# Kernel optimization log

Hardware: AMD Instinct MI355X
Metric: run time of the kernel (lower is better)

## Reference

```python
import jax, jax.numpy as jnp
import numpy as np

B, S, C_IN, C_OUT = 8, 2048, 512, 512

def setup_inputs() -> dict:
    key = jax.random.key(0)
    k1, k2, k3, k4 = jax.random.split(key, 4)
    sc = 1.0 / np.sqrt(C_IN)
    return {
        "x": jax.random.normal(k1, (B, S, C_IN), dtype=jnp.float32),
        "Wq": jax.random.normal(k2, (C_OUT, C_IN), dtype=jnp.float32) * sc,
        "Wk": jax.random.normal(k3, (C_OUT, C_IN), dtype=jnp.float32) * sc,
        "Wv": jax.random.normal(k4, (C_OUT, C_IN), dtype=jnp.float32) * sc,
    }

def reference(x, Wq, Wk, Wv):
    # x: [B,S,Cin]; weights [Cout,Cin] (torch Linear convention, no bias)
    C = Wq.shape[0]
    dk = jnp.sqrt(jnp.float32(1.0) / C)  # torch: sqrt(1/out_features)
    q = jnp.einsum('bsi,oi->bso', x, Wq)
    k = jnp.einsum('bsi,oi->bso', x, Wk)
    v = jnp.einsum('bsi,oi->bso', x, Wv)
    phi_q = jax.nn.elu(q * dk) + 1.0
    phi_k = jax.nn.elu(k * dk) + 1.0
    b = x.shape[0]
    mem0 = jnp.zeros((b, C, C), x.dtype)   # running sum of phi_k v^T
    zeta0 = jnp.zeros((b, C), x.dtype)     # running sum of phi_k
    def step(carry, inp):
        mem, zeta = carry
        pq, pk, vv = inp                    # each [B,C]
        dm = pk[:, :, None] * vv[:, None, :]              # [B,C,C]
        scale = jnp.einsum('bc,bc->b', pq, pk + zeta) + 1e-5
        num = jnp.einsum('bc,bcd->bd', pq, dm + mem)
        y = num / scale[:, None]
        # state updates are under torch.no_grad -> detach
        new_mem = jax.lax.stop_gradient(mem + dm)
        new_zeta = jax.lax.stop_gradient(zeta + pk)
        return (new_mem, new_zeta), y
    xs = (phi_q.transpose(1, 0, 2), phi_k.transpose(1, 0, 2), v.transpose(1, 0, 2))
    _, ys = jax.lax.scan(step, (mem0, zeta0), xs)  # ys: [S,B,C]
    return ys.transpose(1, 0, 2)                   # [B,S,C]
```

## Files before the change

### kernel.cpp

```cpp
#include <hip/hip_runtime.h>


constexpr int Bn  = 8;
constexpr int Sn  = 2048;
constexpr int Cn  = 512;
constexpr int Tn  = 128;
constexpr int NCn = 16;
constexpr float DKf = 0.04419417382415922f;

typedef __attribute__((ext_vector_type(8))) short bf16x8;
typedef __attribute__((ext_vector_type(4))) float f32x4;

__device__ __forceinline__ unsigned short f2bf(float f) {
  unsigned u = __float_as_uint(f);
  u = (u + 0x7fffu + ((u >> 16) & 1u)) >> 16;
  return (unsigned short)u;
}
__device__ __forceinline__ float bf2f(unsigned short h) {
  return __uint_as_float(((unsigned)h) << 16);
}
__device__ __forceinline__ float phi_f(float u) {
  float s = u * DKf;
  return s > 0.0f ? s + 1.0f : __expf(s);
}

__global__ __launch_bounds__(256) void k_cast(
    const float* __restrict__ x, const float* __restrict__ Wq,
    const float* __restrict__ Wk, const float* __restrict__ Wv,
    unsigned short* __restrict__ xb, unsigned short* __restrict__ Wb)
{
  const int bid = blockIdx.x;
  const float* src;
  unsigned short* dst;
  size_t i8;
  if (bid < 4096) {
    i8 = ((size_t)bid * 256 + threadIdx.x) * 8;
    src = x; dst = xb;
  } else {
    const size_t f = ((size_t)(bid - 4096) * 256 + threadIdx.x) * 8;
    const int z = (int)(f >> 18);
    src = (z == 0) ? Wq : (z == 1 ? Wk : Wv);
    dst = Wb + ((size_t)z << 18);
    i8 = f & ((1u << 18) - 1);
  }
  float4 a = *(const float4*)&src[i8];
  float4 b = *(const float4*)&src[i8 + 4];
  uint4 o;
  o.x = (unsigned)f2bf(a.x) | ((unsigned)f2bf(a.y) << 16);
  o.y = (unsigned)f2bf(a.z) | ((unsigned)f2bf(a.w) << 16);
  o.z = (unsigned)f2bf(b.x) | ((unsigned)f2bf(b.y) << 16);
  o.w = (unsigned)f2bf(b.z) | ((unsigned)f2bf(b.w) << 16);
  *(uint4*)&dst[i8] = o;
}

__device__ __forceinline__ void stage128x64(const unsigned short* __restrict__ g,
                                            int ld, unsigned short* lds,
                                            int wid, int lane) {
#pragma unroll
  for (int e = 0; e < 4; ++e) {
    const int row = e * 32 + wid * 8 + (lane >> 3);
    const int ks  = (lane & 7) ^ (row & 7);
    const unsigned short* src = g + (size_t)row * ld + ks * 8;
    unsigned short* dst = lds + (size_t)(e * 256 + wid * 64) * 8;
    __builtin_amdgcn_global_load_lds(
        (const __attribute__((address_space(1))) void*)src,
        (__attribute__((address_space(3))) void*)dst, 16, 0, 0);
  }
}

__global__ __launch_bounds__(256) void k_proj(
    const unsigned short* __restrict__ xb, const unsigned short* __restrict__ Wb,
    unsigned short* __restrict__ PQ, unsigned short* __restrict__ PK,
    unsigned short* __restrict__ PKt, unsigned short* __restrict__ Vt,
    float* __restrict__ zsum)
{
  __shared__ unsigned short Al[2 * 8192], Bl[2 * 8192];
  __shared__ float zbuf[2][128];
  const int bid = blockIdx.x;
  const int xcd = bid & 7, idx = bid >> 3;
  const int n = idx & 3, z = (idx >> 2) % 3, mloc = idx / 12;
  const int n0 = n * 128, m0 = (xcd * 16 + mloc) * 128;
  const int t = threadIdx.x, wid = t >> 6, lane = t & 63;
  const int wm = wid >> 1, wn = wid & 1;
  const int fr = lane & 15, kb = lane >> 4;
  f32x4 acc[4][4];
  const f32x4 zero = {0.f, 0.f, 0.f, 0.f};
#pragma unroll
  for (int m = 0; m < 4; ++m)
#pragma unroll
    for (int nn = 0; nn < 4; ++nn) acc[m][nn] = zero;

  const unsigned short* Ag = xb + (size_t)m0 * Cn;
  const unsigned short* Bg = Wb + (size_t)z * Cn * Cn + (size_t)n0 * Cn;

  stage128x64(Ag, Cn, Al, wid, lane);
  stage128x64(Bg, Cn, Bl, wid, lane);
  int cur = 0;
  for (int kt = 0; kt < 8; ++kt) {
    const int nxt = cur ^ 1;
    if (kt + 1 < 8) {
      stage128x64(Ag + (kt + 1) * 64, Cn, Al + nxt * 8192, wid, lane);
      stage128x64(Bg + (kt + 1) * 64, Cn, Bl + nxt * 8192, wid, lane);
      asm volatile("s_waitcnt vmcnt(8)" ::: "memory");
    } else {
      asm volatile("s_waitcnt vmcnt(0)" ::: "memory");
    }
    __builtin_amdgcn_s_barrier();
    asm volatile("" ::: "memory");
    const unsigned short* Ac = Al + cur * 8192;
    const unsigned short* Bc = Bl + cur * 8192;
#pragma unroll
    for (int kk = 0; kk < 2; ++kk) {
      bf16x8 af[4], bf[4];
#pragma unroll
      for (int m = 0; m < 4; ++m) {
        const int r = wm * 64 + m * 16 + fr;
        af[m] = *(const bf16x8*)&Ac[r * 64 + (((kk * 4 + kb) ^ (r & 7)) << 3)];
      }
#pragma unroll
      for (int nn = 0; nn < 4; ++nn) {
        const int r = wn * 64 + nn * 16 + fr;
        bf[nn] = *(const bf16x8*)&Bc[r * 64 + (((kk * 4 + kb) ^ (r & 7)) << 3)];
      }
      __builtin_amdgcn_s_setprio(1);
#pragma unroll
      for (int m = 0; m < 4; ++m)
#pragma unroll
        for (int nn = 0; nn < 4; ++nn)
          acc[m][nn] = __builtin_amdgcn_mfma_f32_16x16x32_bf16(af[m], bf[nn], acc[m][nn], 0, 0, 0);
      __builtin_amdgcn_s_setprio(0);
    }
    __builtin_amdgcn_s_barrier();
    asm volatile("" ::: "memory");
    cur = nxt;
  }

  float ps[4] = {0.f, 0.f, 0.f, 0.f};
#pragma unroll
  for (int m = 0; m < 4; ++m)
#pragma unroll
    for (int nn = 0; nn < 4; ++nn) {
      const int row0 = m0 + wm * 64 + m * 16 + ((lane >> 4) << 2);
      const int col  = n0 + wn * 64 + nn * 16 + fr;
      f32x4 v = acc[m][nn];
      if (z == 0) {
#pragma unroll
        for (int j = 0; j < 4; ++j)
          PQ[(size_t)(row0 + j) * Cn + col] = f2bf(phi_f(v[j]));
      } else if (z == 1) {
        ushort4 p;
#pragma unroll
        for (int j = 0; j < 4; ++j) {
          unsigned short u = f2bf(phi_f(v[j]));
          PK[(size_t)(row0 + j) * Cn + col] = u;
          (&p.x)[j] = u;
          ps[nn] += bf2f(u);
        }
        const int b = row0 >> 11, tq = row0 & (Sn - 1);
        *(ushort4*)&PKt[((size_t)b * Cn + col) * Sn + tq] = p;
      } else {
        ushort4 p;
#pragma unroll
        for (int j = 0; j < 4; ++j) (&p.x)[j] = f2bf(v[j]);
        const int b = row0 >> 11, tq = row0 & (Sn - 1);
        *(ushort4*)&Vt[((size_t)b * Cn + col) * Sn + tq] = p;
      }
    }

  if (z == 1) {
#pragma unroll
    for (int nn = 0; nn < 4; ++nn) {
      float v = ps[nn];
      v += __shfl_xor(v, 16); v += __shfl_xor(v, 32);
      if (lane < 16) zbuf[wm][wn * 64 + nn * 16 + lane] = v;
    }
    __syncthreads();
    if (t < 128) {
      const int b = m0 >> 11, ch = (m0 >> 7) & 15;
      zsum[((size_t)b * NCn + ch) * Cn + n0 + t] = zbuf[0][t] + zbuf[1][t];
    }
  }
}

__device__ __forceinline__ void stageA64(const unsigned short* __restrict__ g,
                                         unsigned short* lds, int wid, int lane) {
  const int row = wid * 16 + (lane >> 2);
  const int ks  = (lane & 3) ^ ((row >> 1) & 3);
  __builtin_amdgcn_global_load_lds(
      (const __attribute__((address_space(1))) void*)(g + (size_t)row * Cn + ks * 8),
      (__attribute__((address_space(3))) void*)(lds + wid * 512), 16, 0, 0);
}
__device__ __forceinline__ void stageB128(const unsigned short* __restrict__ g,
                                          unsigned short* lds, int wid, int lane) {
#pragma unroll
  for (int e = 0; e < 2; ++e) {
    const int row = e * 64 + wid * 16 + (lane >> 2);
    const int ks  = (lane & 3) ^ ((row >> 1) & 3);
    __builtin_amdgcn_global_load_lds(
        (const __attribute__((address_space(1))) void*)(g + (size_t)row * Cn + ks * 8),
        (__attribute__((address_space(3))) void*)(lds + e * 2048 + wid * 512),
        16, 0, 0);
  }
}

__device__ __forceinline__ void stage64x128(const unsigned short* __restrict__ g,
                                            int ld, unsigned short* lds,
                                            int wid, int lane) {
#pragma unroll
  for (int i = 0; i < 4; ++i) {
    const int row = wid * 16 + i * 4 + (lane >> 4);
    const int s   = (lane & 15) ^ (row & 7);
    const unsigned short* src = g + (size_t)row * ld + s * 8;
    unsigned short* dst = lds + (size_t)(wid * 16 + i * 4) * 128;
    __builtin_amdgcn_global_load_lds(
        (const __attribute__((address_space(1))) void*)src,
        (__attribute__((address_space(3))) void*)dst, 16, 0, 0);
  }
}

__global__ __launch_bounds__(256) void k_gk(
    const unsigned short* __restrict__ PQ, const unsigned short* __restrict__ PK,
    const float* __restrict__ zsum,
    unsigned short* __restrict__ Abuf, float* __restrict__ scale,
    const unsigned short* __restrict__ PKt, const unsigned short* __restrict__ Vt,
    unsigned short* __restrict__ Mpre)
{
  __shared__ unsigned short smem[32768];
  const int t = threadIdx.x, wid = t >> 6, lane = t & 63;
  const int fr = lane & 15, kb = lane >> 4;
  const f32x4 zero = {0.f, 0.f, 0.f, 0.f};

  if (blockIdx.x < 512) {
    unsigned short* Al = smem;
    unsigned short* Bl = smem + 16384;
    const int bid = blockIdx.x;
    const int b = bid & 7, idx = bid >> 3;
    const int d0 = (idx & 7) * 64, c0 = (idx >> 3) * 64;
    const int wm = wid >> 1, wn = wid & 1;
    f32x4 acc[2][2];
#pragma unroll
    for (int m = 0; m < 2; ++m)
#pragma unroll
      for (int n = 0; n < 2; ++n) acc[m][n] = zero;
    const unsigned short* Ag = PKt + ((size_t)b * Cn + c0) * Sn;
    const unsigned short* Bg = Vt  + ((size_t)b * Cn + d0) * Sn;
    stage64x128(Ag, Sn, Al, wid, lane);
    stage64x128(Bg, Sn, Bl, wid, lane);
    int cur = 0;
    for (int ch = 0; ch < NCn; ++ch) {
      const int nxt = cur ^ 1;
      if (ch + 1 < NCn) {
        stage64x128(Ag + (ch + 1) * Tn, Sn, Al + nxt * 8192, wid, lane);
        stage64x128(Bg + (ch + 1) * Tn, Sn, Bl + nxt * 8192, wid, lane);
        asm volatile("s_waitcnt vmcnt(8)" ::: "memory");
      } else {
        asm volatile("s_waitcnt vmcnt(0)" ::: "memory");
      }
      __builtin_amdgcn_s_barrier();
      asm volatile("" ::: "memory");
      if (ch > 0) {
#pragma unroll
        for (int m = 0; m < 2; ++m)
#pragma unroll
          for (int n = 0; n < 2; ++n) {
            const int c_row = c0 + wm * 32 + m * 16 + (kb << 2);
            const int d     = d0 + wn * 32 + n * 16 + fr;
            ushort4 p;
#pragma unroll
            for (int j = 0; j < 4; ++j) (&p.x)[j] = f2bf(acc[m][n][j]);
            *(ushort4*)&Mpre[((size_t)(b * NCn + ch) * Cn + d) * Cn + c_row] = p;
          }
      }
      const unsigned short* Ac = Al + cur * 8192;
      const unsigned short* Bc = Bl + cur * 8192;
      __builtin_amdgcn_s_setprio(1);
#pragma unroll
      for (int kt = 0; kt < 4; ++kt) {
        bf16x8 af[2], bf[2];
#pragma unroll
        for (int m = 0; m < 2; ++m) {
          const int r = wm * 32 + m * 16 + fr;
          af[m] = *(const bf16x8*)&Ac[r * 128 + (((kt * 4 + kb) ^ (r & 7)) << 3)];
        }
#pragma unroll
        for (int n = 0; n < 2; ++n) {
          const int r = wn * 32 + n * 16 + fr;
          bf[n] = *(const bf16x8*)&Bc[r * 128 + (((kt * 4 + kb) ^ (r & 7)) << 3)];
        }
#pragma unroll
        for (int m = 0; m < 2; ++m)
#pragma unroll
          for (int n = 0; n < 2; ++n)
            acc[m][n] = __builtin_amdgcn_mfma_f32_16x16x32_bf16(af[m], bf[n], acc[m][n], 0, 0, 0);
      }
      __builtin_amdgcn_s_setprio(0);
      __builtin_amdgcn_s_barrier();
      asm volatile("" ::: "memory");
      cur = nxt;
    }
  } else {
    unsigned short* Asl = smem;
    unsigned short* Bsl = smem + 6144;
    float* rsmem = (float*)(smem + 18432);
    float* zpl   = rsmem + 256;
    const int g = blockIdx.x - 512;
    const int i0 = (g & 1) * 64, ch = (g >> 1) & 15, b = g >> 5;
    const unsigned short* Aq = PQ + ((size_t)(b * Sn + ch * Tn + i0)) * Cn;
    const unsigned short* Bk = PK + ((size_t)(b * Sn + ch * Tn)) * Cn;
    f32x4 acc[4][2];
#pragma unroll
    for (int m = 0; m < 4; ++m)
#pragma unroll
      for (int n = 0; n < 2; ++n) acc[m][n] = zero;

    stageA64(Aq, Asl, wid, lane);
    stageB128(Bk, Bsl, wid, lane);
    stageA64(Aq + 32, Asl + 2048, wid, lane);
    stageB128(Bk + 32, Bsl + 4096, wid, lane);
    int cur = 0;
    for (int kt = 0; kt < 16; ++kt) {
      if (kt + 2 < 16) {
        const int nx2 = (cur + 2 >= 3) ? cur - 1 : cur + 2;
        stageA64(Aq + (kt + 2) * 32, Asl + nx2 * 2048, wid, lane);
        stageB128(Bk + (kt + 2) * 32, Bsl + nx2 * 4096, wid, lane);
        asm volatile("s_waitcnt vmcnt(6)" ::: "memory");
      } else if (kt + 1 < 16) {
        asm volatile("s_waitcnt vmcnt(3)" ::: "memory");
      } else {
        asm volatile("s_waitcnt vmcnt(0)" ::: "memory");
      }
      __builtin_amdgcn_s_barrier();
      asm volatile("" ::: "memory");
      const unsigned short* Ac = Asl + cur * 2048;
      const unsigned short* Bc = Bsl + cur * 4096;
      bf16x8 af[4], bf[2];
#pragma unroll
      for (int m = 0; m < 4; ++m) {
        const int r = m * 16 + fr;
        af[m] = *(const bf16x8*)&Ac[r * 32 + ((kb ^ ((r >> 1) & 3)) << 3)];
      }
#pragma unroll
      for (int n = 0; n < 2; ++n) {
        const int c = wid * 32 + n * 16 + fr;
        bf[n] = *(const bf16x8*)&Bc[c * 32 + ((kb ^ ((c >> 1) & 3)) << 3)];
      }
      __builtin_amdgcn_s_setprio(1);
#pragma unroll
      for (int m = 0; m < 4; ++m)
#pragma unroll
        for (int n = 0; n < 2; ++n)
          acc[m][n] = __builtin_amdgcn_mfma_f32_16x16x32_bf16(af[m], bf[n], acc[m][n], 0, 0, 0);
      __builtin_amdgcn_s_setprio(0);
      __builtin_amdgcn_s_barrier();
      asm volatile("" ::: "memory");
      cur = (cur + 1 >= 3) ? 0 : cur + 1;
    }

    float rsum[4][4];
#pragma unroll
    for (int m = 0; m < 4; ++m)
#pragma unroll
      for (int j = 0; j < 4; ++j) rsum[m][j] = 0.f;
#pragma unroll
    for (int m = 0; m < 4; ++m)
#pragma unroll
      for (int n = 0; n < 2; ++n) {
        f32x4 v = acc[m][n];
#pragma unroll
        for (int j = 0; j < 4; ++j) {
          const int row_g = i0 + m * 16 + kb * 4 + j;
          const int col   = wid * 32 + n * 16 + fr;
          unsigned short u = (col <= row_g) ? f2bf(v[j]) : 0;
          Abuf[((size_t)(b * NCn + ch) * Tn + row_g) * Tn + col] = u;
          rsum[m][j] += bf2f(u);
        }
      }
#pragma unroll
    for (int m = 0; m < 4; ++m)
#pragma unroll
      for (int j = 0; j < 4; ++j) {
        float r = rsum[m][j];
        r += __shfl_xor(r, 1); r += __shfl_xor(r, 2);
        r += __shfl_xor(r, 4); r += __shfl_xor(r, 8);
        if (fr == 0) rsmem[wid * 64 + m * 16 + kb * 4 + j] = r;
      }
#pragma unroll
    for (int e = 0; e < 2; ++e) {
      const int c = t + e * 256;
      float s = 0.f;
      for (int ch2 = 0; ch2 < ch; ++ch2)
        s += zsum[((size_t)b * NCn + ch2) * Cn + c];
      zpl[c] = s;
    }
    __syncthreads();
    const int row = t >> 2, q4 = (t & 3) * 128;
    const unsigned short* pq = Aq + (size_t)row * Cn + q4;
    float dacc = 0.f;
    for (int i = 0; i < 128; i += 8) {
      uint4 q = *(const uint4*)(pq + i);
      dacc += bf2f((unsigned short)(q.x & 0xffff)) * zpl[q4 + i + 0]
            + bf2f((unsigned short)(q.x >> 16))    * zpl[q4 + i + 1]
            + bf2f((unsigned short)(q.y & 0xffff)) * zpl[q4 + i + 2]
            + bf2f((unsigned short)(q.y >> 16))    * zpl[q4 + i + 3]
            + bf2f((unsigned short)(q.z & 0xffff)) * zpl[q4 + i + 4]
            + bf2f((unsigned short)(q.z >> 16))    * zpl[q4 + i + 5]
            + bf2f((unsigned short)(q.w & 0xffff)) * zpl[q4 + i + 6]
            + bf2f((unsigned short)(q.w >> 16))    * zpl[q4 + i + 7];
    }
    dacc += __shfl_xor(dacc, 1);
    dacc += __shfl_xor(dacc, 2);
    if ((t & 3) == 0)
      scale[(size_t)b * Sn + ch * Tn + i0 + row] =
          rsmem[0 * 64 + row] + rsmem[1 * 64 + row] +
          rsmem[2 * 64 + row] + rsmem[3 * 64 + row] + dacc + 1e-5f;
  }
}

__device__ __forceinline__ void stage128x32(const unsigned short* __restrict__ g,
                                            int ld, unsigned short* lds,
                                            int wid, int lane) {
#pragma unroll
  for (int cc = 0; cc < 2; ++cc) {
    const int row = cc * 64 + wid * 16 + (lane >> 2);
    const int ks  = (lane & 3) ^ ((row >> 1) & 3);
    const unsigned short* src = g + (size_t)row * ld + ks * 8;
    unsigned short* dst = lds + (size_t)(cc * 256 + wid * 64) * 8;
    __builtin_amdgcn_global_load_lds(
        (const __attribute__((address_space(1))) void*)src,
        (__attribute__((address_space(3))) void*)dst, 16, 0, 0);
  }
}

__global__ __launch_bounds__(256) void k_avinter(
    const unsigned short* __restrict__ Abuf, const unsigned short* __restrict__ Vt,
    const unsigned short* __restrict__ PQ, const unsigned short* __restrict__ Mpre,
    const float* __restrict__ scale, float* __restrict__ out)
{
  __shared__ unsigned short Al[3 * 128 * 32], Bl[3 * 128 * 32];
  const int bid = blockIdx.x;
  const int logical = (bid & 7) * 64 + (bid >> 3);
  const int d0 = (logical & 3) * 128;
  const int ch = (logical >> 2) & 15;
  const int b  = logical >> 6;
  const int t0 = ch * Tn;
  const int t = threadIdx.x, wid = t >> 6, lane = t & 63;
  const int wm = wid >> 1, wn = wid & 1;
  const int fr = lane & 15, kb = lane >> 4;
  f32x4 acc[4][4];
  const f32x4 zero = {0.f, 0.f, 0.f, 0.f};
#pragma unroll
  for (int m = 0; m < 4; ++m)
#pragma unroll
    for (int n = 0; n < 4; ++n) acc[m][n] = zero;

  const unsigned short* Aintra = Abuf + (size_t)(b * NCn + ch) * Tn * Tn;
  const unsigned short* Bintra = Vt + ((size_t)b * Cn + d0) * Sn + t0;
  const unsigned short* Ainter = PQ + ((size_t)b * Sn + t0) * Cn;
  const unsigned short* Binter = Mpre + ((size_t)(b * NCn + ch) * Cn + d0) * Cn;
  auto srcA = [&](int kt) { return (kt < 4) ? Aintra + kt * 32 : Ainter + (kt - 4) * 32; };
  auto srcB = [&](int kt) { return (kt < 4) ? Bintra + kt * 32 : Binter + (kt - 4) * 32; };
  auto ldA  = [&](int kt) { return (kt < 4) ? Tn : Cn; };
  auto ldB  = [&](int kt) { return (kt < 4) ? Sn : Cn; };
  const int nkt = (ch > 0) ? 20 : 4;

  stage128x32(srcA(0), ldA(0), Al, wid, lane);
  stage128x32(srcB(0), ldB(0), Bl, wid, lane);
  stage128x32(srcA(1), ldA(1), Al + 4096, wid, lane);
  stage128x32(srcB(1), ldB(1), Bl + 4096, wid, lane);
  int cur = 0;
  for (int kt = 0; kt < nkt; ++kt) {
    if (kt + 2 < nkt) {
      const int nx2 = (cur + 2 >= 3) ? cur - 1 : cur + 2;
      stage128x32(srcA(kt + 2), ldA(kt + 2), Al + nx2 * 4096, wid, lane);
      stage128x32(srcB(kt + 2), ldB(kt + 2), Bl + nx2 * 4096, wid, lane);
      asm volatile("s_waitcnt vmcnt(8)" ::: "memory");
    } else if (kt + 1 < nkt) {
      asm volatile("s_waitcnt vmcnt(4)" ::: "memory");
    } else {
      asm volatile("s_waitcnt vmcnt(0)" ::: "memory");
    }
    __builtin_amdgcn_s_barrier();
    asm volatile("" ::: "memory");
    const unsigned short* Ac = Al + cur * 4096;
    const unsigned short* Bc = Bl + cur * 4096;
    bf16x8 af[4], bf[4];
#pragma unroll
    for (int m = 0; m < 4; ++m) {
      const int r = wm * 64 + m * 16 + fr;
      af[m] = *(const bf16x8*)&Ac[r * 32 + ((kb ^ ((r >> 1) & 3)) << 3)];
    }
#pragma unroll
    for (int n = 0; n < 4; ++n) {
      const int r = wn * 64 + n * 16 + fr;
      bf[n] = *(const bf16x8*)&Bc[r * 32 + ((kb ^ ((r >> 1) & 3)) << 3)];
    }
    __builtin_amdgcn_s_setprio(1);
#pragma unroll
    for (int m = 0; m < 4; ++m)
#pragma unroll
      for (int n = 0; n < 4; ++n)
        acc[m][n] = __builtin_amdgcn_mfma_f32_16x16x32_bf16(af[m], bf[n], acc[m][n], 0, 0, 0);
    __builtin_amdgcn_s_setprio(0);
    __builtin_amdgcn_s_barrier();
    asm volatile("" ::: "memory");
    cur = (cur + 1 >= 3) ? 0 : cur + 1;
  }

#pragma unroll
  for (int m = 0; m < 4; ++m)
#pragma unroll
    for (int n = 0; n < 4; ++n) {
      const int row0 = t0 + wm * 64 + m * 16 + ((lane >> 4) << 2);
      const int col  = d0 + wn * 64 + n * 16 + (lane & 15);
      f32x4 v = acc[m][n];
#pragma unroll
      for (int j = 0; j < 4; ++j) {
        const size_t sidx = (size_t)b * Sn + row0 + j;
        out[sidx * Cn + col] = v[j] / scale[sidx];
      }
    }
}

extern "C" void kernel_launch(void* const* d_in, const int* in_sizes, int n_in,
                              void* d_out, int out_size, void* d_ws, size_t ws_size,
                              hipStream_t stream)
{
  const float* x  = (const float*)d_in[0];
  const float* Wq = (const float*)d_in[1];
  const float* Wk = (const float*)d_in[2];
  const float* Wv = (const float*)d_in[3];
  float* out = (float*)d_out;

  unsigned short* xb   = (unsigned short*)d_ws;
  unsigned short* Wb   = xb   + (size_t)Bn * Sn * Cn;
  unsigned short* PQ   = Wb   + (size_t)3 * Cn * Cn;
  unsigned short* PK   = PQ   + (size_t)Bn * Sn * Cn;
  unsigned short* PKt  = PK   + (size_t)Bn * Sn * Cn;
  unsigned short* Vt   = PKt  + (size_t)Bn * Sn * Cn;
  unsigned short* Abuf = Vt   + (size_t)Bn * Sn * Cn;
  unsigned short* Mpre = Abuf + (size_t)Bn * NCn * Tn * Tn;
  float* scale = (float*)(Mpre + (size_t)Bn * NCn * Cn * Cn);
  float* zsum  = scale + (size_t)Bn * Sn;
  (void)ws_size; (void)in_sizes; (void)n_in; (void)out_size;

  hipLaunchKernelGGL(k_cast, dim3(4096 + 384), dim3(256), 0, stream, x, Wq, Wk, Wv, xb, Wb);
  hipLaunchKernelGGL(k_proj, dim3(1536), dim3(256), 0, stream, xb, Wb, PQ, PK, PKt, Vt, zsum);
  hipLaunchKernelGGL(k_gk, dim3(768), dim3(256), 0, stream,
                     PQ, PK, zsum, Abuf, scale, PKt, Vt, Mpre);
  hipLaunchKernelGGL(k_avinter, dim3(512), dim3(256), 0, stream, Abuf, Vt, PQ, Mpre, scale, out);
}
```

Before: 118.3 us.

## Fuse x fp32-to-bf16 conversion into projection GEMM A-tile loading

```diff
diff --git a/kernel.cpp b/kernel.cpp
--- a/kernel.cpp
+++ b/kernel.cpp
@@ -23,34 +23,26 @@
   float s = u * DKf;
   return s > 0.0f ? s + 1.0f : __expf(s);
 }
-
-__global__ __launch_bounds__(256) void k_cast(
-    const float* __restrict__ x, const float* __restrict__ Wq,
-    const float* __restrict__ Wk, const float* __restrict__ Wv,
-    unsigned short* __restrict__ xb, unsigned short* __restrict__ Wb)
-{
-  const int bid = blockIdx.x;
-  const float* src;
-  unsigned short* dst;
-  size_t i8;
-  if (bid < 4096) {
-    i8 = ((size_t)bid * 256 + threadIdx.x) * 8;
-    src = x; dst = xb;
-  } else {
-    const size_t f = ((size_t)(bid - 4096) * 256 + threadIdx.x) * 8;
-    const int z = (int)(f >> 18);
-    src = (z == 0) ? Wq : (z == 1 ? Wk : Wv);
-    dst = Wb + ((size_t)z << 18);
-    i8 = f & ((1u << 18) - 1);
-  }
-  float4 a = *(const float4*)&src[i8];
-  float4 b = *(const float4*)&src[i8 + 4];
+__device__ __forceinline__ uint4 pack8(const float4 a, const float4 b) {
   uint4 o;
   o.x = (unsigned)f2bf(a.x) | ((unsigned)f2bf(a.y) << 16);
   o.y = (unsigned)f2bf(a.z) | ((unsigned)f2bf(a.w) << 16);
   o.z = (unsigned)f2bf(b.x) | ((unsigned)f2bf(b.y) << 16);
   o.w = (unsigned)f2bf(b.z) | ((unsigned)f2bf(b.w) << 16);
-  *(uint4*)&dst[i8] = o;
+  return o;
+}
+
+__global__ __launch_bounds__(256) void k_castw(
+    const float* __restrict__ Wq, const float* __restrict__ Wk,
+    const float* __restrict__ Wv, unsigned short* __restrict__ Wb)
+{
+  const size_t f = ((size_t)blockIdx.x * 256 + threadIdx.x) * 8;
+  const int z = (int)(f >> 18);
+  const float* __restrict__ src = (z == 0) ? Wq : (z == 1 ? Wk : Wv);
+  const size_t i8 = f & ((1u << 18) - 1);
+  float4 a = *(const float4*)&src[i8];
+  float4 b = *(const float4*)&src[i8 + 4];
+  *(uint4*)&Wb[((size_t)z << 18) + i8] = pack8(a, b);
 }
 
 __device__ __forceinline__ void stage128x64(const unsigned short* __restrict__ g,
@@ -69,7 +61,7 @@
 }
 
 __global__ __launch_bounds__(256) void k_proj(
-    const unsigned short* __restrict__ xb, const unsigned short* __restrict__ Wb,
+    const float* __restrict__ xf, const unsigned short* __restrict__ Wb,
     unsigned short* __restrict__ PQ, unsigned short* __restrict__ PK,
     unsigned short* __restrict__ PKt, unsigned short* __restrict__ Vt,
     float* __restrict__ zsum)
@@ -90,21 +82,39 @@
 #pragma unroll
     for (int nn = 0; nn < 4; ++nn) acc[m][nn] = zero;
 
-  const unsigned short* Ag = xb + (size_t)m0 * Cn;
+  const int arow = t >> 3;
+  const int acs  = t & 7;
+  const float* xp = xf + (size_t)(m0 + arow) * Cn + acs * 8;
+  const int awoff = arow * 64 + (((acs ^ (arow & 7)) & 7) << 3);
   const unsigned short* Bg = Wb + (size_t)z * Cn * Cn + (size_t)n0 * Cn;
 
-  stage128x64(Ag, Cn, Al, wid, lane);
+  float4 a0[4], a1[4];
+#pragma unroll
+  for (int e = 0; e < 4; ++e) {
+    a0[e] = *(const float4*)(xp + (size_t)e * 32 * Cn);
+    a1[e] = *(const float4*)(xp + (size_t)e * 32 * Cn + 4);
+  }
   stage128x64(Bg, Cn, Bl, wid, lane);
+
   int cur = 0;
   for (int kt = 0; kt < 8; ++kt) {
     const int nxt = cur ^ 1;
+    unsigned short* bufA = Al + cur * 8192;
+#pragma unroll
+    for (int e = 0; e < 4; ++e)
+      *(uint4*)&bufA[awoff + e * 2048] = pack8(a0[e], a1[e]);
     if (kt + 1 < 8) {
-      stage128x64(Ag + (kt + 1) * 64, Cn, Al + nxt * 8192, wid, lane);
+#pragma unroll
+      for (int e = 0; e < 4; ++e) {
+        a0[e] = *(const float4*)(xp + (size_t)e * 32 * Cn + (kt + 1) * 64);
+        a1[e] = *(const float4*)(xp + (size_t)e * 32 * Cn + (kt + 1) * 64 + 4);
+      }
       stage128x64(Bg + (kt + 1) * 64, Cn, Bl + nxt * 8192, wid, lane);
-      asm volatile("s_waitcnt vmcnt(8)" ::: "memory");
+      asm volatile("s_waitcnt vmcnt(12)" ::: "memory");
     } else {
       asm volatile("s_waitcnt vmcnt(0)" ::: "memory");
     }
+    asm volatile("s_waitcnt lgkmcnt(0)" ::: "memory");
     __builtin_amdgcn_s_barrier();
     asm volatile("" ::: "memory");
     const unsigned short* Ac = Al + cur * 8192;
@@ -531,8 +541,7 @@
   const float* Wv = (const float*)d_in[3];
   float* out = (float*)d_out;
 
-  unsigned short* xb   = (unsigned short*)d_ws;
-  unsigned short* Wb   = xb   + (size_t)Bn * Sn * Cn;
+  unsigned short* Wb   = (unsigned short*)d_ws;
   unsigned short* PQ   = Wb   + (size_t)3 * Cn * Cn;
   unsigned short* PK   = PQ   + (size_t)Bn * Sn * Cn;
   unsigned short* PKt  = PK   + (size_t)Bn * Sn * Cn;
@@ -543,8 +552,8 @@
   float* zsum  = scale + (size_t)Bn * Sn;
   (void)ws_size; (void)in_sizes; (void)n_in; (void)out_size;
 
-  hipLaunchKernelGGL(k_cast, dim3(4096 + 384), dim3(256), 0, stream, x, Wq, Wk, Wv, xb, Wb);
-  hipLaunchKernelGGL(k_proj, dim3(1536), dim3(256), 0, stream, xb, Wb, PQ, PK, PKt, Vt, zsum);
+  hipLaunchKernelGGL(k_castw, dim3(384), dim3(256), 0, stream, Wq, Wk, Wv, Wb);
+  hipLaunchKernelGGL(k_proj, dim3(1536), dim3(256), 0, stream, x, Wb, PQ, PK, PKt, Vt, zsum);
   hipLaunchKernelGGL(k_gk, dim3(768), dim3(256), 0, stream,
                      PQ, PK, zsum, Abuf, scale, PKt, Vt, Mpre);
   hipLaunchKernelGGL(k_avinter, dim3(512), dim3(256), 0, stream, Abuf, Vt, PQ, Mpre, scale, out);
```

Result: slower. 128.7 us (+8.8%).
